# Optimization experiments

Measured on AMD Instinct MI355X. Metric: run time of the kernel, lower is better.

## Reference

```python
import jax, jax.numpy as jnp
import numpy as np

LN_EPS = 1e-5

def setup_inputs() -> dict:
    key = jax.random.key(0)
    ks = jax.random.split(key, 4)
    B, T, N, D, G = 8, 48, 1024, 64, 256
    x = jax.random.normal(ks[0], (B, T, N, D), dtype=jnp.float32)
    view = jax.random.uniform(ks[1], (G, N), dtype=jnp.float32)
    w = jax.random.normal(ks[2], (N, D, D), dtype=jnp.float32) * 0.02
    b = jax.random.normal(ks[3], (1, N, D), dtype=jnp.float32) * 0.02
    gamma = jnp.ones((D,), dtype=jnp.float32)
    beta = jnp.zeros((D,), dtype=jnp.float32)
    return {"x": x, "view": view, "w": w, "b": b, "gamma": gamma, "beta": beta}

def _layernorm(x, gamma, beta):
    mu = jnp.mean(x, axis=-1, keepdims=True)
    var = jnp.mean(jnp.square(x - mu), axis=-1, keepdims=True)
    return (x - mu) * jax.lax.rsqrt(var + LN_EPS) * gamma + beta

def reference(x, view, w, b, gamma, beta):
    # per-node linear transform: [B,T,N,D] x [N,D,D] -> [B,T,N,D]
    h = jnp.einsum('btni,nio->btno', x, w)
    h = h + b[0]  # bias broadcast over batch and time
    # grid aggregation via view mapping: [B,T,N,D] x [G,N] -> [B,T,G,D]
    g = jnp.einsum('btnd,gn->btgd', h, view)
    return _layernorm(g, gamma, beta)
```

## Files before the change

kernel.cpp:

```cpp
#include <hip/hip_runtime.h>
#include <stdint.h>
#include <stddef.h>


#define LNEPS 1e-5f

typedef __attribute__((ext_vector_type(8))) short bf16x8;
typedef __attribute__((ext_vector_type(4))) float f32x4;
typedef union { unsigned u[4]; bf16x8 v; } fragu;

static __device__ __forceinline__ unsigned rne(unsigned u) {
    return u + 0x7FFFu + ((u >> 16) & 1u);
}
static __device__ __forceinline__ void split_pair(float a, float b,
                                                  unsigned& hw_, unsigned& lw_) {
    unsigned ra = rne(__float_as_uint(a));
    unsigned rb = rne(__float_as_uint(b));
    hw_ = (ra >> 16) | (rb & 0xFFFF0000u);
    float fa = a - __uint_as_float(ra & 0xFFFF0000u);
    float fb = b - __uint_as_float(rb & 0xFFFF0000u);
    unsigned sa = rne(__float_as_uint(fa));
    unsigned sb = rne(__float_as_uint(fb));
    lw_ = (sa >> 16) | (sb & 0xFFFF0000u);
}
static __device__ __forceinline__ unsigned packhl(float vv) {
    unsigned r = rne(__float_as_uint(vv));
    unsigned hif = r & 0xFFFF0000u;
    float res = vv - __uint_as_float(hif);
    unsigned s = rne(__float_as_uint(res));
    return hif | (s >> 16);
}

static __device__ __forceinline__ void gll16(const void* g, void* l) {
    __builtin_amdgcn_global_load_lds(
        (const __attribute__((address_space(1))) void*)g,
        (__attribute__((address_space(3))) void*)l, 16, 0, 0);
}

#define WS_H   0u
#define WS_VH  100663296u
#define WS_VL  101187584u
#define WS_VB  101711872u

__global__ __launch_bounds__(256) void k0_prep(
        const float* __restrict__ view, const float* __restrict__ bias,
        unsigned short* __restrict__ vh, unsigned short* __restrict__ vl,
        float* __restrict__ vb) {
    const int g = blockIdx.x;
    const int tid = threadIdx.x;
    float4 vv = *(const float4*)(view + g * 1024 + tid * 4);
    unsigned h01, l01, h23, l23;
    split_pair(vv.x, vv.y, h01, l01);
    split_pair(vv.z, vv.w, h23, l23);
    *(uint2*)(vh + g * 1024 + tid * 4) = make_uint2(h01, h23);
    *(uint2*)(vl + g * 1024 + tid * 4) = make_uint2(l01, l23);
    const int q = tid >> 6, d = tid & 63;
    const float* vrow = view + g * 1024;
    float a = 0.f;
    #pragma unroll 8
    for (int nn = q * 256; nn < q * 256 + 256; ++nn)
        a = fmaf(vrow[nn], bias[nn * 64 + d], a);
    __shared__ float red[4][64];
    red[q][d] = a;
    __syncthreads();
    if (tid < 64)
        vb[g * 64 + tid] = red[0][tid] + red[1][tid] + red[2][tid] + red[3][tid];
}

__global__ __launch_bounds__(1024) void k1_node(
        const float* __restrict__ x, const float* __restrict__ w,
        unsigned char* __restrict__ hb) {
    __shared__ unsigned T[16 * 16 * 68];
    const int tid = threadIdx.x;
    const int l  = tid & 63, wv = tid >> 6;
    const int lc = l & 15,  lg = l >> 4;
    const int ng = blockIdx.x & 63, btg = blockIdx.x >> 6;
    const int n0 = ng * 16, bt_base = btg * 96;
    const int n = n0 + wv;

    bf16x8 bh[4][2], bl[4][2];
    #pragma unroll
    for (int cs = 0; cs < 4; ++cs) {
        #pragma unroll
        for (int kc = 0; kc < 2; ++kc) {
            const float* wp = w + (size_t)n * 4096 + (size_t)(kc * 32 + lg * 8) * 64
                                + cs * 16 + lc;
            float e[8];
            #pragma unroll
            for (int j = 0; j < 8; ++j) e[j] = wp[(size_t)j * 64];
            fragu H, L;
            #pragma unroll
            for (int k2 = 0; k2 < 4; ++k2)
                split_pair(e[2 * k2], e[2 * k2 + 1], H.u[k2], L.u[k2]);
            bh[cs][kc] = H.v;
            bl[cs][kc] = L.v;
        }
    }

    const int btl = tid >> 6;
    const int dT  = tid & 63;

    for (int t = 0; t < 6; ++t) {
        const float* xp = x + (size_t)(bt_base + t * 16 + lc) * 65536u
                            + (size_t)n * 64 + lg * 8;
        float4 x0 = *(const float4*)(xp);
        float4 x1 = *(const float4*)(xp + 4);
        float4 x2 = *(const float4*)(xp + 32);
        float4 x3 = *(const float4*)(xp + 36);

        bf16x8 ah[2], al[2];
        {
            fragu H, L;
            split_pair(x0.x, x0.y, H.u[0], L.u[0]);
            split_pair(x0.z, x0.w, H.u[1], L.u[1]);
            split_pair(x1.x, x1.y, H.u[2], L.u[2]);
            split_pair(x1.z, x1.w, H.u[3], L.u[3]);
            ah[0] = H.v; al[0] = L.v;
        }
        {
            fragu H, L;
            split_pair(x2.x, x2.y, H.u[0], L.u[0]);
            split_pair(x2.z, x2.w, H.u[1], L.u[1]);
            split_pair(x3.x, x3.y, H.u[2], L.u[2]);
            split_pair(x3.z, x3.w, H.u[3], L.u[3]);
            ah[1] = H.v; al[1] = L.v;
        }

        f32x4 acc[4];
        #pragma unroll
        for (int cs = 0; cs < 4; ++cs) acc[cs] = (f32x4){0.f, 0.f, 0.f, 0.f};
        #pragma unroll
        for (int cs = 0; cs < 4; ++cs) {
            #pragma unroll
            for (int kc = 0; kc < 2; ++kc) {
                acc[cs] = __builtin_amdgcn_mfma_f32_16x16x32_bf16(ah[kc], bh[cs][kc], acc[cs], 0, 0, 0);
                acc[cs] = __builtin_amdgcn_mfma_f32_16x16x32_bf16(ah[kc], bl[cs][kc], acc[cs], 0, 0, 0);
                acc[cs] = __builtin_amdgcn_mfma_f32_16x16x32_bf16(al[kc], bh[cs][kc], acc[cs], 0, 0, 0);
                acc[cs] = __builtin_amdgcn_mfma_f32_16x16x32_bf16(al[kc], bl[cs][kc], acc[cs], 0, 0, 0);
            }
        }
        #pragma unroll
        for (int cs = 0; cs < 4; ++cs) {
            #pragma unroll
            for (int j = 0; j < 4; ++j)
                T[wv * 1088 + (lg * 4 + j) * 68 + cs * 16 + lc] = packhl(acc[cs][j]);
        }
        asm volatile("s_waitcnt lgkmcnt(0)" ::: "memory");
        __builtin_amdgcn_s_barrier();

        {
            unsigned vv[16];
            #pragma unroll
            for (int nn = 0; nn < 16; ++nn) vv[nn] = T[nn * 1088 + btl * 68 + dT];
            unsigned hd[8], ld[8];
            #pragma unroll
            for (int k = 0; k < 8; ++k) {
                hd[k] = (vv[2 * k] >> 16) | (vv[2 * k + 1] & 0xFFFF0000u);
                ld[k] = (vv[2 * k] & 0xFFFFu) | (vv[2 * k + 1] << 16);
            }
            unsigned char* dst = hb + (size_t)(bt_base + t * 16 + btl) * 262144u
                                    + (size_t)dT * 4096u + ng * 64;
            ((uint4*)dst)[0] = make_uint4(hd[0], hd[1], hd[2], hd[3]);
            ((uint4*)dst)[1] = make_uint4(hd[4], hd[5], hd[6], hd[7]);
            ((uint4*)dst)[2] = make_uint4(ld[0], ld[1], ld[2], ld[3]);
            ((uint4*)dst)[3] = make_uint4(ld[4], ld[5], ld[6], ld[7]);
        }
        asm volatile("s_waitcnt lgkmcnt(0)" ::: "memory");
        __builtin_amdgcn_s_barrier();
    }
}

#define KB2 24576

__global__ __launch_bounds__(256, 3) void k2_grid(
        const unsigned short* __restrict__ vh, const unsigned short* __restrict__ vl,
        const unsigned char* __restrict__ hb, const float* __restrict__ vb,
        const float* __restrict__ gamma, const float* __restrict__ beta,
        float* __restrict__ out) {
    __shared__ __align__(16) unsigned char smem[2 * KB2];
    const int tid = threadIdx.x;
    const int l  = tid & 63;
    const int wv = tid >> 6;
    const int b  = blockIdx.x;
    const int bm = (b >> 3) & 1;
    const int bt = (b & 7) + (b >> 4) * 8;
    const int lc = l & 15, lg = l >> 4;

    const unsigned short* a_src[4];
    int a_dst[4];
    #pragma unroll
    for (int c = 0; c < 4; ++c) {
        int id = (wv * 4 + c) * 64 + l;
        int row = id >> 3;
        int slot = id & 7;
        int sg = slot ^ (row & 7);
        int plg = sg >> 2, kcg = sg & 3;
        const unsigned short* pl = plg ? vl : vh;
        a_src[c] = pl + (size_t)(bm * 128 + row) * 1024 + kcg * 8;
        a_dst[c] = (wv * 4 + c) * 1024;
    }
    const unsigned char* b_src[2];
    int b_dst[2];
    #pragma unroll
    for (int c = 0; c < 2; ++c) {
        int id = (wv * 2 + c) * 64 + l;
        int d_ = id >> 3;
        int slot = id & 7;
        int sg = slot ^ (d_ & 7);
        b_src[c] = hb + (size_t)bt * 262144u + (size_t)d_ * 4096u
                      + (sg >> 2) * 64 + ((sg >> 1) & 1) * 32 + (sg & 1) * 16;
        b_dst[c] = 16384 + (wv * 2 + c) * 1024;
    }
    int aoff[2][2];
    #pragma unroll
    for (int st = 0; st < 2; ++st)
        #pragma unroll
        for (int pl = 0; pl < 2; ++pl) {
            int row = wv * 32 + st * 16 + lc;
            aoff[st][pl] = row * 128 + ((((pl << 2) | lg) ^ (row & 7)) * 16);
        }
    int boff[4][2];
    #pragma unroll
    for (int cs = 0; cs < 4; ++cs)
        #pragma unroll
        for (int pl = 0; pl < 2; ++pl) {
            int d_ = cs * 16 + lc;
            int sg = ((lg >> 1) << 2) | (pl << 1) | (lg & 1);
            boff[cs][pl] = 16384 + d_ * 128 + ((sg ^ (d_ & 7)) * 16);
        }

    f32x4 acc[2][4];
    #pragma unroll
    for (int st = 0; st < 2; ++st)
        #pragma unroll
        for (int cs = 0; cs < 4; ++cs)
            acc[st][cs] = (f32x4){0.f, 0.f, 0.f, 0.f};

#define K2_STAGE(KB, S) do {                                                  \
    _Pragma("unroll")                                                         \
    for (int c_ = 0; c_ < 4; ++c_)                                            \
        gll16(a_src[c_] + (size_t)(S) * 32, smem + (KB) + a_dst[c_]);         \
    _Pragma("unroll")                                                         \
    for (int c_ = 0; c_ < 2; ++c_)                                            \
        gll16(b_src[c_] + (size_t)(S) * 128, smem + (KB) + b_dst[c_]);        \
} while (0)

    K2_STAGE(0, 0);
    int kb = 0;
    for (int s = 0; s < 32; ++s) {
        if (s < 31) {
            K2_STAGE(kb ^ KB2, s + 1);
            asm volatile("s_waitcnt vmcnt(6)" ::: "memory");
        } else {
            asm volatile("s_waitcnt vmcnt(0)" ::: "memory");
        }
        __builtin_amdgcn_s_barrier();
        bf16x8 a0h = *(const bf16x8*)(smem + kb + aoff[0][0]);
        bf16x8 a0l = *(const bf16x8*)(smem + kb + aoff[0][1]);
        bf16x8 a1h = *(const bf16x8*)(smem + kb + aoff[1][0]);
        bf16x8 a1l = *(const bf16x8*)(smem + kb + aoff[1][1]);
        #pragma unroll
        for (int cs = 0; cs < 4; ++cs) {
            bf16x8 bhf = *(const bf16x8*)(smem + kb + boff[cs][0]);
            bf16x8 blf = *(const bf16x8*)(smem + kb + boff[cs][1]);
            acc[0][cs] = __builtin_amdgcn_mfma_f32_16x16x32_bf16(a0h, bhf, acc[0][cs], 0, 0, 0);
            acc[0][cs] = __builtin_amdgcn_mfma_f32_16x16x32_bf16(a0h, blf, acc[0][cs], 0, 0, 0);
            acc[0][cs] = __builtin_amdgcn_mfma_f32_16x16x32_bf16(a0l, bhf, acc[0][cs], 0, 0, 0);
            acc[1][cs] = __builtin_amdgcn_mfma_f32_16x16x32_bf16(a1h, bhf, acc[1][cs], 0, 0, 0);
            acc[1][cs] = __builtin_amdgcn_mfma_f32_16x16x32_bf16(a1h, blf, acc[1][cs], 0, 0, 0);
            acc[1][cs] = __builtin_amdgcn_mfma_f32_16x16x32_bf16(a1l, bhf, acc[1][cs], 0, 0, 0);
        }
        __builtin_amdgcn_s_barrier();
        kb ^= KB2;
    }

    float gam[4], bet[4];
    #pragma unroll
    for (int cs = 0; cs < 4; ++cs) {
        gam[cs] = gamma[cs * 16 + lc];
        bet[cs] = beta[cs * 16 + lc];
    }
    #pragma unroll
    for (int st = 0; st < 2; ++st) {
        #pragma unroll
        for (int j = 0; j < 4; ++j) {
            int g = bm * 128 + wv * 32 + st * 16 + lg * 4 + j;
            float v[4];
            float s1 = 0.f, s2 = 0.f;
            #pragma unroll
            for (int cs = 0; cs < 4; ++cs) {
                v[cs] = acc[st][cs][j] + vb[g * 64 + cs * 16 + lc];
                s1 += v[cs];
                s2 += v[cs] * v[cs];
            }
            s1 += __shfl_xor(s1, 1);  s2 += __shfl_xor(s2, 1);
            s1 += __shfl_xor(s1, 2);  s2 += __shfl_xor(s2, 2);
            s1 += __shfl_xor(s1, 4);  s2 += __shfl_xor(s2, 4);
            s1 += __shfl_xor(s1, 8);  s2 += __shfl_xor(s2, 8);
            float mu  = s1 * 0.015625f;
            float var = s2 * 0.015625f - mu * mu;
            float inv = rsqrtf(var + LNEPS);
            size_t ob = (size_t)bt * 16384u + (size_t)g * 64u;
            #pragma unroll
            for (int cs = 0; cs < 4; ++cs)
                out[ob + cs * 16 + lc] = (v[cs] - mu) * inv * gam[cs] + bet[cs];
        }
    }
#undef K2_STAGE
}

extern "C" void kernel_launch(void* const* d_in, const int* in_sizes, int n_in,
                              void* d_out, int out_size, void* d_ws, size_t ws_size,
                              hipStream_t stream) {
    (void)in_sizes; (void)n_in; (void)out_size; (void)ws_size;
    const float* x     = (const float*)d_in[0];
    const float* view  = (const float*)d_in[1];
    const float* w     = (const float*)d_in[2];
    const float* bias  = (const float*)d_in[3];
    const float* gamma = (const float*)d_in[4];
    const float* beta  = (const float*)d_in[5];
    float* out = (float*)d_out;

    char* ws = (char*)d_ws;
    unsigned char* hb  = (unsigned char*)(ws + WS_H);
    unsigned short* vh = (unsigned short*)(ws + WS_VH);
    unsigned short* vl = (unsigned short*)(ws + WS_VL);
    float* vb          = (float*)(ws + WS_VB);

    hipLaunchKernelGGL(k0_prep, dim3(256), dim3(256), 0, stream,
                       view, bias, vh, vl, vb);
    hipLaunchKernelGGL(k1_node, dim3(256), dim3(1024), 0, stream, x, w, hb);
    hipLaunchKernelGGL(k2_grid, dim3(768), dim3(256), 0, stream,
                       vh, vl, hb, vb, gamma, beta, out);
}
```

Before: 271.9 us.

## Store intermediate in MFMA fragment order so grid GEMM loads directly from global

The node kernel now writes the split bf16 hi/lo intermediate in a layout where each lane's MFMA B fragment is a contiguous 32-byte chunk. This lets the grid kernel drop its LDS double-buffered global_load_lds pipeline and barriers and load A/B fragments straight from global memory. The node kernel also moves to 512-thread blocks over 8 nodes and 48 timesteps, with the next x tile prefetched into registers. Dropping LDS staging removes sync overhead, but it relies on cache hits for the reused view fragments and loses the explicit overlap of loads with compute.

```diff
diff --git a/kernel.cpp b/kernel.cpp
--- a/kernel.cpp
+++ b/kernel.cpp
@@ -29,12 +29,6 @@
     float res = vv - __uint_as_float(hif);
     unsigned s = rne(__float_as_uint(res));
     return hif | (s >> 16);
-}
-
-static __device__ __forceinline__ void gll16(const void* g, void* l) {
-    __builtin_amdgcn_global_load_lds(
-        (const __attribute__((address_space(1))) void*)g,
-        (__attribute__((address_space(3))) void*)l, 16, 0, 0);
 }
 
 #define WS_H   0u
@@ -67,15 +61,15 @@
         vb[g * 64 + tid] = red[0][tid] + red[1][tid] + red[2][tid] + red[3][tid];
 }
 
-__global__ __launch_bounds__(1024) void k1_node(
+__global__ __launch_bounds__(512) void k1_node(
         const float* __restrict__ x, const float* __restrict__ w,
         unsigned char* __restrict__ hb) {
-    __shared__ unsigned T[16 * 16 * 68];
+    __shared__ unsigned T[8 * 16 * 68];
     const int tid = threadIdx.x;
     const int l  = tid & 63, wv = tid >> 6;
     const int lc = l & 15,  lg = l >> 4;
-    const int ng = blockIdx.x & 63, btg = blockIdx.x >> 6;
-    const int n0 = ng * 16, bt_base = btg * 96;
+    const int ng = blockIdx.x & 127, btg = blockIdx.x >> 7;
+    const int n0 = ng * 8, bt_base = btg * 48;
     const int n = n0 + wv;
 
     bf16x8 bh[4][2], bl[4][2];
@@ -97,33 +91,44 @@
         }
     }
 
-    const int btl = tid >> 6;
+    const int btl0 = tid >> 6;
     const int dT  = tid & 63;
 
-    for (int t = 0; t < 6; ++t) {
-        const float* xp = x + (size_t)(bt_base + t * 16 + lc) * 65536u
+    float4 xq[4];
+    {
+        const float* xp = x + (size_t)(bt_base + lc) * 65536u
                             + (size_t)n * 64 + lg * 8;
-        float4 x0 = *(const float4*)(xp);
-        float4 x1 = *(const float4*)(xp + 4);
-        float4 x2 = *(const float4*)(xp + 32);
-        float4 x3 = *(const float4*)(xp + 36);
-
+        xq[0] = *(const float4*)(xp);
+        xq[1] = *(const float4*)(xp + 4);
+        xq[2] = *(const float4*)(xp + 32);
+        xq[3] = *(const float4*)(xp + 36);
+    }
+
+    for (int t = 0; t < 3; ++t) {
         bf16x8 ah[2], al[2];
         {
             fragu H, L;
-            split_pair(x0.x, x0.y, H.u[0], L.u[0]);
-            split_pair(x0.z, x0.w, H.u[1], L.u[1]);
-            split_pair(x1.x, x1.y, H.u[2], L.u[2]);
-            split_pair(x1.z, x1.w, H.u[3], L.u[3]);
+            split_pair(xq[0].x, xq[0].y, H.u[0], L.u[0]);
+            split_pair(xq[0].z, xq[0].w, H.u[1], L.u[1]);
+            split_pair(xq[1].x, xq[1].y, H.u[2], L.u[2]);
+            split_pair(xq[1].z, xq[1].w, H.u[3], L.u[3]);
             ah[0] = H.v; al[0] = L.v;
         }
         {
             fragu H, L;
-            split_pair(x2.x, x2.y, H.u[0], L.u[0]);
-            split_pair(x2.z, x2.w, H.u[1], L.u[1]);
-            split_pair(x3.x, x3.y, H.u[2], L.u[2]);
-            split_pair(x3.z, x3.w, H.u[3], L.u[3]);
+            split_pair(xq[2].x, xq[2].y, H.u[0], L.u[0]);
+            split_pair(xq[2].z, xq[2].w, H.u[1], L.u[1]);
+            split_pair(xq[3].x, xq[3].y, H.u[2], L.u[2]);
+            split_pair(xq[3].z, xq[3].w, H.u[3], L.u[3]);
             ah[1] = H.v; al[1] = L.v;
+        }
+        if (t < 2) {
+            const float* xp = x + (size_t)(bt_base + (t + 1) * 16 + lc) * 65536u
+                                + (size_t)n * 64 + lg * 8;
+            xq[0] = *(const float4*)(xp);
+            xq[1] = *(const float4*)(xp + 4);
+            xq[2] = *(const float4*)(xp + 32);
+            xq[3] = *(const float4*)(xp + 36);
         }
 
         f32x4 acc[4];
@@ -148,36 +153,33 @@
         asm volatile("s_waitcnt lgkmcnt(0)" ::: "memory");
         __builtin_amdgcn_s_barrier();
 
-        {
-            unsigned vv[16];
-            #pragma unroll
-            for (int nn = 0; nn < 16; ++nn) vv[nn] = T[nn * 1088 + btl * 68 + dT];
-            unsigned hd[8], ld[8];
-            #pragma unroll
-            for (int k = 0; k < 8; ++k) {
+        #pragma unroll
+        for (int half = 0; half < 2; ++half) {
+            int btl = btl0 + half * 8;
+            unsigned vv[8];
+            #pragma unroll
+            for (int nn = 0; nn < 8; ++nn) vv[nn] = T[nn * 1088 + btl * 68 + dT];
+            unsigned hd[4], ld[4];
+            #pragma unroll
+            for (int k = 0; k < 4; ++k) {
                 hd[k] = (vv[2 * k] >> 16) | (vv[2 * k + 1] & 0xFFFF0000u);
                 ld[k] = (vv[2 * k] & 0xFFFFu) | (vv[2 * k + 1] << 16);
             }
             unsigned char* dst = hb + (size_t)(bt_base + t * 16 + btl) * 262144u
-                                    + (size_t)dT * 4096u + ng * 64;
+                                    + (size_t)ng * 2048u + dT * 32;
             ((uint4*)dst)[0] = make_uint4(hd[0], hd[1], hd[2], hd[3]);
-            ((uint4*)dst)[1] = make_uint4(hd[4], hd[5], hd[6], hd[7]);
-            ((uint4*)dst)[2] = make_uint4(ld[0], ld[1], ld[2], ld[3]);
-            ((uint4*)dst)[3] = make_uint4(ld[4], ld[5], ld[6], ld[7]);
+            ((uint4*)dst)[1] = make_uint4(ld[0], ld[1], ld[2], ld[3]);
         }
         asm volatile("s_waitcnt lgkmcnt(0)" ::: "memory");
         __builtin_amdgcn_s_barrier();
     }
 }
-
-#define KB2 24576
 
 __global__ __launch_bounds__(256, 3) void k2_grid(
         const unsigned short* __restrict__ vh, const unsigned short* __restrict__ vl,
         const unsigned char* __restrict__ hb, const float* __restrict__ vb,
         const float* __restrict__ gamma, const float* __restrict__ beta,
         float* __restrict__ out) {
-    __shared__ __align__(16) unsigned char smem[2 * KB2];
     const int tid = threadIdx.x;
     const int l  = tid & 63;
     const int wv = tid >> 6;
@@ -186,48 +188,9 @@
     const int bt = (b & 7) + (b >> 4) * 8;
     const int lc = l & 15, lg = l >> 4;
 
-    const unsigned short* a_src[4];
-    int a_dst[4];
-    #pragma unroll
-    for (int c = 0; c < 4; ++c) {
-        int id = (wv * 4 + c) * 64 + l;
-        int row = id >> 3;
-        int slot = id & 7;
-        int sg = slot ^ (row & 7);
-        int plg = sg >> 2, kcg = sg & 3;
-        const unsigned short* pl = plg ? vl : vh;
-        a_src[c] = pl + (size_t)(bm * 128 + row) * 1024 + kcg * 8;
-        a_dst[c] = (wv * 4 + c) * 1024;
-    }
-    const unsigned char* b_src[2];
-    int b_dst[2];
-    #pragma unroll
-    for (int c = 0; c < 2; ++c) {
-        int id = (wv * 2 + c) * 64 + l;
-        int d_ = id >> 3;
-        int slot = id & 7;
-        int sg = slot ^ (d_ & 7);
-        b_src[c] = hb + (size_t)bt * 262144u + (size_t)d_ * 4096u
-                      + (sg >> 2) * 64 + ((sg >> 1) & 1) * 32 + (sg & 1) * 16;
-        b_dst[c] = 16384 + (wv * 2 + c) * 1024;
-    }
-    int aoff[2][2];
-    #pragma unroll
-    for (int st = 0; st < 2; ++st)
-        #pragma unroll
-        for (int pl = 0; pl < 2; ++pl) {
-            int row = wv * 32 + st * 16 + lc;
-            aoff[st][pl] = row * 128 + ((((pl << 2) | lg) ^ (row & 7)) * 16);
-        }
-    int boff[4][2];
-    #pragma unroll
-    for (int cs = 0; cs < 4; ++cs)
-        #pragma unroll
-        for (int pl = 0; pl < 2; ++pl) {
-            int d_ = cs * 16 + lc;
-            int sg = ((lg >> 1) << 2) | (pl << 1) | (lg & 1);
-            boff[cs][pl] = 16384 + d_ * 128 + ((sg ^ (d_ & 7)) * 16);
-        }
+    const unsigned short* aH = vh + (size_t)(bm * 128 + wv * 32 + lc) * 1024 + lg * 8;
+    const unsigned short* aL = vl + (size_t)(bm * 128 + wv * 32 + lc) * 1024 + lg * 8;
+    const unsigned char* bb = hb + (size_t)bt * 262144u + lg * 2048 + lc * 32;
 
     f32x4 acc[2][4];
     #pragma unroll
@@ -236,33 +199,17 @@
         for (int cs = 0; cs < 4; ++cs)
             acc[st][cs] = (f32x4){0.f, 0.f, 0.f, 0.f};
 
-#define K2_STAGE(KB, S) do {                                                  \
-    _Pragma("unroll")                                                         \
-    for (int c_ = 0; c_ < 4; ++c_)                                            \
-        gll16(a_src[c_] + (size_t)(S) * 32, smem + (KB) + a_dst[c_]);         \
-    _Pragma("unroll")                                                         \
-    for (int c_ = 0; c_ < 2; ++c_)                                            \
-        gll16(b_src[c_] + (size_t)(S) * 128, smem + (KB) + b_dst[c_]);        \
-} while (0)
-
-    K2_STAGE(0, 0);
-    int kb = 0;
+    #pragma unroll 4
     for (int s = 0; s < 32; ++s) {
-        if (s < 31) {
-            K2_STAGE(kb ^ KB2, s + 1);
-            asm volatile("s_waitcnt vmcnt(6)" ::: "memory");
-        } else {
-            asm volatile("s_waitcnt vmcnt(0)" ::: "memory");
-        }
-        __builtin_amdgcn_s_barrier();
-        bf16x8 a0h = *(const bf16x8*)(smem + kb + aoff[0][0]);
-        bf16x8 a0l = *(const bf16x8*)(smem + kb + aoff[0][1]);
-        bf16x8 a1h = *(const bf16x8*)(smem + kb + aoff[1][0]);
-        bf16x8 a1l = *(const bf16x8*)(smem + kb + aoff[1][1]);
+        bf16x8 a0h = *(const bf16x8*)(aH + s * 32);
+        bf16x8 a0l = *(const bf16x8*)(aL + s * 32);
+        bf16x8 a1h = *(const bf16x8*)(aH + 16384 + s * 32);
+        bf16x8 a1l = *(const bf16x8*)(aL + 16384 + s * 32);
+        const unsigned char* bp = bb + (size_t)s * 8192u;
         #pragma unroll
         for (int cs = 0; cs < 4; ++cs) {
-            bf16x8 bhf = *(const bf16x8*)(smem + kb + boff[cs][0]);
-            bf16x8 blf = *(const bf16x8*)(smem + kb + boff[cs][1]);
+            bf16x8 bhf = *(const bf16x8*)(bp + cs * 512);
+            bf16x8 blf = *(const bf16x8*)(bp + cs * 512 + 16);
             acc[0][cs] = __builtin_amdgcn_mfma_f32_16x16x32_bf16(a0h, bhf, acc[0][cs], 0, 0, 0);
             acc[0][cs] = __builtin_amdgcn_mfma_f32_16x16x32_bf16(a0h, blf, acc[0][cs], 0, 0, 0);
             acc[0][cs] = __builtin_amdgcn_mfma_f32_16x16x32_bf16(a0l, bhf, acc[0][cs], 0, 0, 0);
@@ -270,8 +217,6 @@
             acc[1][cs] = __builtin_amdgcn_mfma_f32_16x16x32_bf16(a1h, blf, acc[1][cs], 0, 0, 0);
             acc[1][cs] = __builtin_amdgcn_mfma_f32_16x16x32_bf16(a1l, bhf, acc[1][cs], 0, 0, 0);
         }
-        __builtin_amdgcn_s_barrier();
-        kb ^= KB2;
     }
 
     float gam[4], bet[4];
@@ -306,7 +251,6 @@
                 out[ob + cs * 16 + lc] = (v[cs] - mu) * inv * gam[cs] + bet[cs];
         }
     }
-#undef K2_STAGE
 }
 
 extern "C" void kernel_launch(void* const* d_in, const int* in_sizes, int n_in,
@@ -329,7 +273,7 @@
 
     hipLaunchKernelGGL(k0_prep, dim3(256), dim3(256), 0, stream,
                        view, bias, vh, vl, vb);
-    hipLaunchKernelGGL(k1_node, dim3(256), dim3(1024), 0, stream, x, w, hb);
+    hipLaunchKernelGGL(k1_node, dim3(1024), dim3(512), 0, stream, x, w, hb);
     hipLaunchKernelGGL(k2_grid, dim3(768), dim3(256), 0, stream,
                        vh, vl, hb, vb, gamma, beta, out);
 }
```

New measurement: 274.8 us. About the same (+1.1%).
